# Performance work log

Measured on AMD Instinct MI355X. Metric: run time of the kernel, lower is better.

The kernel has to match this reference:

```python
import jax, jax.numpy as jnp
import numpy as np

B, H, W, C = 4, 64, 64, 256       # C == number_of_filters // 2
NOF = 512
CA = NOF // 8                      # f/g projection dim = 64
CH = NOF // 2                      # h / output projection dim = 256 (== C)


def setup_inputs() -> dict:
    key = jax.random.key(0)
    ks = jax.random.split(key, 10)
    sc = 1.0 / np.sqrt(C)
    x = jax.random.normal(ks[0], (B, H, W, C), jnp.float32)
    Wf = jax.random.normal(ks[1], (C, CA), jnp.float32) * sc
    bf = jnp.zeros((CA,), jnp.float32)
    Wg = jax.random.normal(ks[2], (C, CA), jnp.float32) * sc
    bg = jnp.zeros((CA,), jnp.float32)
    Wh = jax.random.normal(ks[3], (C, CH), jnp.float32) * sc
    bh = jnp.zeros((CH,), jnp.float32)
    Wo = jax.random.normal(ks[4], (CH, CH), jnp.float32) * (1.0 / np.sqrt(CH))
    bo = jnp.zeros((CH,), jnp.float32)
    gamma = jax.random.normal(ks[5], (1,), jnp.float32) * 0.1
    return {"x": x, "Wf": Wf, "bf": bf, "Wg": Wg, "bg": bg,
            "Wh": Wh, "bh": bh, "Wo": Wo, "bo": bo, "gamma": gamma}


def reference(x, Wf, bf, Wg, bg, Wh, bh, Wo, bo, gamma):
    b, h, w, c = x.shape
    n = h * w
    # 1x1 conv projections == per-pixel matmuls over channels
    f = (jnp.einsum('bhwc,cd->bhwd', x, Wf) + bf).reshape(b, n, -1)   # [B,N,CA]
    g = (jnp.einsum('bhwc,cd->bhwd', x, Wg) + bg).reshape(b, n, -1)   # [B,N,CA]
    hh = (jnp.einsum('bhwc,cd->bhwd', x, Wh) + bh).reshape(b, n, -1)  # [B,N,CH]
    # s = g @ f^T : full spatial attention scores [B,N,N]
    s = jnp.einsum('bnd,bmd->bnm', g, f)
    beta = jax.nn.softmax(s, axis=-1)
    o = jnp.einsum('bnm,bmc->bnc', beta, hh).reshape(b, h, w, c)      # CH == C
    # post-attention 1x1 conv
    o2 = jnp.einsum('bhwc,cd->bhwd', o, Wo) + bo
    y = gamma * o2 + x
    return y
```

## Files before the change

kernel.cpp:

```cpp
#include <hip/hip_runtime.h>

typedef __bf16  bf16x8 __attribute__((ext_vector_type(8)));
typedef short   s16x8  __attribute__((ext_vector_type(8)));
typedef float   f32x4  __attribute__((ext_vector_type(4)));
typedef float   f32x16 __attribute__((ext_vector_type(16)));
typedef int     i32x2  __attribute__((ext_vector_type(2)));
typedef int     i32x4  __attribute__((ext_vector_type(4)));

#define LOG2E 1.44269504088896f
#define SM_M2 (44.0f * LOG2E)

__device__ __forceinline__ unsigned short f2bf(float f){
  unsigned u = __builtin_bit_cast(unsigned, f);
  return (unsigned short)((u + 0x7fffu + ((u >> 16) & 1u)) >> 16);
}

__device__ __forceinline__ int cvtpk_bf16(float a, float b){
  int r; asm("v_cvt_pk_bf16_f32 %0, %1, %2" : "=v"(r) : "v"(a), "v"(b)); return r;
}

__device__ __forceinline__ float bfhalf2f(unsigned short u){
  unsigned v = ((unsigned)u) << 16; return __builtin_bit_cast(float, v);
}

#define OFF_WTFG 0u
#define OFF_WHT  65536u
#define OFF_WOT  196608u
#define OFF_F    8716288u
#define OFF_G    10813440u
#define OFF_HT   12910592u
#define OFF_PART 21299200u
#define OFF_LP   38076416u

__global__ __launch_bounds__(256) void prep(const float* __restrict__ Wf, const float* __restrict__ Wg,
                                            const float* __restrict__ Wh, const float* __restrict__ Wo,
                                            unsigned short* __restrict__ WTfg,
                                            unsigned short* __restrict__ WhT,
                                            unsigned short* __restrict__ WoT){
  int t = blockIdx.x * 256 + threadIdx.x;
  if (t < 32768) {
    int n = t >> 8, k = t & 255;
    float v = (n < 64) ? Wf[k * 64 + n] : Wg[k * 64 + (n - 64)];
    WTfg[t] = f2bf(v);
  } else if (t < 98304) {
    int i = t - 32768; int n = i >> 8, k = i & 255;
    WhT[i] = f2bf(Wh[k * 256 + n]);
  } else {
    int i = t - 98304; int n = i >> 8, k = i & 255;
    WoT[i] = f2bf(Wo[k * 256 + n]);
  }
}

__global__ __launch_bounds__(768) void proj(const float* __restrict__ x,
                                            const unsigned short* __restrict__ WTfg,
                                            const unsigned short* __restrict__ WhT,
                                            const float* __restrict__ bfv, const float* __restrict__ bgv,
                                            const float* __restrict__ bhv,
                                            unsigned short* __restrict__ fK, unsigned short* __restrict__ gQ,
                                            unsigned short* __restrict__ hT){
  __shared__ __attribute__((aligned(16))) char xt[32768];
  const int tid = threadIdx.x;
  const int lane = tid & 63, w = tid >> 6;
  const int l15 = lane & 15, g4 = lane >> 4;
  const int p0 = blockIdx.x * 64;

  for (int c = tid; c < 2048; c += 768) {
    int row = c >> 5, g = c & 31;
    const f32x4* gp = (const f32x4*)(x + (size_t)(p0 + row) * 256 + g * 8);
    f32x4 a = gp[0], bq = gp[1];
    i32x4 u;
    u[0] = cvtpk_bf16(a[0], a[1]);
    u[1] = cvtpk_bf16(a[2], a[3]);
    u[2] = cvtpk_bf16(bq[0], bq[1]);
    u[3] = cvtpk_bf16(bq[2], bq[3]);
    *(i32x4*)(xt + row * 512 + ((g ^ (row & 7)) << 4)) = u;
  }
  __syncthreads();

  auto XFRAG = [&](int pt, int kb) -> bf16x8 {
    int row = pt * 16 + l15;
    return *(const bf16x8*)(xt + row * 512 + (((kb * 4 + g4) ^ (row & 7)) << 4));
  };

  if (w < 4) {
#pragma unroll
    for (int j = 0; j < 2; j++) {
      int ctg = w * 2 + j, c0 = ctg * 16;
      bf16x8 bw[8];
      const unsigned short* wr = WTfg + (c0 + l15) * 256 + g4 * 8;
#pragma unroll
      for (int kb = 0; kb < 8; kb++) bw[kb] = *(const bf16x8*)(wr + kb * 32);
      float bias = (ctg < 4) ? bfv[c0 + l15] : bgv[c0 - 64 + l15];
      unsigned short* outp = (ctg < 4) ? (fK + c0 + l15) : (gQ + (c0 - 64) + l15);
#pragma unroll
      for (int pt = 0; pt < 4; pt++) {
        f32x4 acc = {0.f, 0.f, 0.f, 0.f};
#pragma unroll
        for (int kb = 0; kb < 8; kb++)
          acc = __builtin_amdgcn_mfma_f32_16x16x32_bf16(XFRAG(pt, kb), bw[kb], acc, 0, 0, 0);
#pragma unroll
        for (int r = 0; r < 4; r++) {
          int row = p0 + pt * 16 + g4 * 4 + r;
          outp[row * 64] = f2bf(acc[r] + bias);
        }
      }
    }
  } else {
#pragma unroll
    for (int j = 0; j < 2; j++) {
      int c0 = ((w - 4) * 2 + j) * 16;
      bf16x8 a[8];
      const unsigned short* wr = WhT + (c0 + l15) * 256 + g4 * 8;
#pragma unroll
      for (int kb = 0; kb < 8; kb++) a[kb] = *(const bf16x8*)(wr + kb * 32);
#pragma unroll
      for (int pt = 0; pt < 4; pt++) {
        f32x4 acc = {0.f, 0.f, 0.f, 0.f};
#pragma unroll
        for (int kb = 0; kb < 8; kb++)
          acc = __builtin_amdgcn_mfma_f32_16x16x32_bf16(a[kb], XFRAG(pt, kb), acc, 0, 0, 0);
        int pg = p0 + pt * 16;
        int bq = pg >> 12, n0 = pg & 4095;
        unsigned short* op = hT + bq * (256 * 4096) + n0 + l15;
#pragma unroll
        for (int r = 0; r < 4; r++) {
          int c = c0 + g4 * 4 + r;
          op[c * 4096] = f2bf(acc[r] + bhv[c]);
        }
      }
    }
  }
}

__global__ __launch_bounds__(512, 2) void attn1(const unsigned short* __restrict__ fK,
                                                const unsigned short* __restrict__ gQ,
                                                const unsigned short* __restrict__ hT,
                                                unsigned short* __restrict__ part,
                                                float* __restrict__ lpart){
  __shared__ __attribute__((aligned(16))) char smem[81920];
  const int tid  = threadIdx.x;
  const int lane = tid & 63, w = tid >> 6;
  const int l31  = lane & 31, hi = lane >> 5;
  const int qh   = w >> 1, cs = w & 1;
  const int b    = blockIdx.x & 3;
  const int rest = blockIdx.x >> 2;
  const int qb   = rest >> 1;
  const int kh   = rest & 1;
  const int q0   = qb * 128 + qh * 32;
  const int kbase = kh * 2048;

  const unsigned short* fKb = fK + (size_t)b * 4096 * 64;
  const unsigned short* gQb = gQ + (size_t)b * 4096 * 64;
  const unsigned short* hTb = hT + (size_t)b * 256 * 4096;

  bf16x8 qfr[4];
#pragma unroll
  for (int c4 = 0; c4 < 4; c4++)
    qfr[c4] = *(const bf16x8*)(gQb + (size_t)(q0 + l31) * 64 + c4 * 16 + hi * 8);

  char* buf0 = smem;
  char* buf1 = smem + 32768;
  char* kb0  = smem + 65536;
  char* kb1  = smem + 73728;

  auto STAGE = [&](char* vbuf, char* kbuf, int m0){
    int r = lane >> 3, gl = lane & 7;
#pragma unroll
    for (int k = 0; k < 4; k++){
      int c = 32 * w + k * 8 + r;
      const unsigned short* gp = hTb + (size_t)c * 4096 + m0 + ((gl ^ (c & 7)) * 8);
      __builtin_amdgcn_global_load_lds((const __attribute__((address_space(1))) unsigned int*)gp,
          (__attribute__((address_space(3))) unsigned int*)(vbuf + ((4 * w + k) << 10)), 16, 0, 0);
    }
    {
      int row = 8 * w + r;
      const unsigned short* gp = fKb + (size_t)(m0 + row) * 64 + ((gl ^ r) * 8);
      __builtin_amdgcn_global_load_lds((const __attribute__((address_space(1))) unsigned int*)gp,
          (__attribute__((address_space(3))) unsigned int*)(kbuf + (w << 10)), 16, 0, 0);
    }
  };

  f32x16 acc[4];
#pragma unroll
  for (int ct = 0; ct < 4; ct++)
#pragma unroll
    for (int i = 0; i < 16; i++) acc[ct][i] = 0.f;
  float lvec[16];
#pragma unroll
  for (int i = 0; i < 16; i++) lvec[i] = 0.f;

  auto COMPUTE = [&](const char* kbuf, const char* vbuf){
    bf16x8 Kf[8];
#pragma unroll
    for (int s = 0; s < 2; s++)
#pragma unroll
      for (int c4 = 0; c4 < 4; c4++)
        Kf[s * 4 + c4] = *(const bf16x8*)(kbuf + (s * 32 + l31) * 128 + (((c4 * 2 + hi) ^ (l31 & 7)) << 4));

    f32x16 t0 = {0,0,0,0,0,0,0,0,0,0,0,0,0,0,0,0};
    f32x16 t1 = {0,0,0,0,0,0,0,0,0,0,0,0,0,0,0,0};
#pragma unroll
    for (int c4 = 0; c4 < 4; c4++) t0 = __builtin_amdgcn_mfma_f32_32x32x16_bf16(Kf[c4],     qfr[c4], t0, 0, 0, 0);
#pragma unroll
    for (int c4 = 0; c4 < 4; c4++) t1 = __builtin_amdgcn_mfma_f32_32x32x16_bf16(Kf[4 + c4], qfr[c4], t1, 0, 0, 0);

    float p[32];
#pragma unroll
    for (int r = 0; r < 16; r++) p[r]      = __builtin_amdgcn_exp2f(fmaf(t0[r], LOG2E, -SM_M2));
#pragma unroll
    for (int r = 0; r < 16; r++) p[16 + r] = __builtin_amdgcn_exp2f(fmaf(t1[r], LOG2E, -SM_M2));
#pragma unroll
    for (int r = 0; r < 16; r++) lvec[r] += p[r] + p[16 + r];

    bf16x8 Bf[4];
#pragma unroll
    for (int mc = 0; mc < 4; mc++) {
      int x0 = cvtpk_bf16(p[mc*8+0], p[mc*8+1]);
      int x1 = cvtpk_bf16(p[mc*8+2], p[mc*8+3]);
      int y0 = cvtpk_bf16(p[mc*8+4], p[mc*8+5]);
      int y1 = cvtpk_bf16(p[mc*8+6], p[mc*8+7]);
      int b0, b1, b2, b3;
#if __has_builtin(__builtin_amdgcn_permlane32_swap)
      i32x2 r0 = __builtin_amdgcn_permlane32_swap(x0, y0, false, false);
      i32x2 r1 = __builtin_amdgcn_permlane32_swap(x1, y1, false, false);
      b0 = r0[0]; b1 = r1[0]; b2 = r0[1]; b3 = r1[1];
#else
      int xs0 = __shfl_xor(x0, 32), xs1 = __shfl_xor(x1, 32);
      int ys0 = __shfl_xor(y0, 32), ys1 = __shfl_xor(y1, 32);
      b0 = hi ? ys0 : x0;  b1 = hi ? ys1 : x1;
      b2 = hi ? y0  : xs0; b3 = hi ? y1  : xs1;
#endif
      union { int i[4]; bf16x8 v; } u;
      u.i[0] = b0; u.i[1] = b1; u.i[2] = b2; u.i[3] = b3;
      Bf[mc] = u.v;
    }

#pragma unroll
    for (int mc = 0; mc < 4; mc++) {
#pragma unroll
      for (int ct = 0; ct < 4; ct++) {
        int c = cs * 128 + ct * 32 + l31;
        const char* vp = vbuf + c * 128 + ((((mc * 2 + hi)) ^ (c & 7)) << 4);
        bf16x8 vf = *(const bf16x8*)vp;
        acc[ct] = __builtin_amdgcn_mfma_f32_32x32x16_bf16(vf, Bf[mc], acc[ct], 0, 0, 0);
      }
    }
  };

  STAGE(buf0, kb0, kbase);

  for (int it = 0; it < 32; it += 2) {
    STAGE(buf1, kb1, kbase + (it + 1) * 64);
    asm volatile("s_waitcnt vmcnt(5)" ::: "memory");
    __builtin_amdgcn_sched_barrier(0);
    __builtin_amdgcn_s_barrier();
    __builtin_amdgcn_sched_barrier(0);
    COMPUTE(kb0, buf0);
    __builtin_amdgcn_s_barrier();
    if (it + 2 < 32) {
      STAGE(buf0, kb0, kbase + (it + 2) * 64);
      asm volatile("s_waitcnt vmcnt(5)" ::: "memory");
    } else {
      asm volatile("s_waitcnt vmcnt(0)" ::: "memory");
    }
    __builtin_amdgcn_sched_barrier(0);
    __builtin_amdgcn_s_barrier();
    __builtin_amdgcn_sched_barrier(0);
    COMPUTE(kb1, buf1);
    __builtin_amdgcn_s_barrier();
  }

  float l_part = 0.f;
#pragma unroll
  for (int r = 0; r < 16; r++) l_part += lvec[r];
  l_part += __shfl_xor(l_part, 32);

  size_t tile = (size_t)((b * 32 + qb) * 2 + kh);
  if (cs == 0 && hi == 0)
    lpart[tile * 128 + qh * 32 + l31] = l_part;

  unsigned short* pbase = part + tile * (128 * 256);
  char* obase = smem;
#pragma unroll 1
  for (int ch = 0; ch < 4; ch++) {
    __syncthreads();
    if (qh == ch) {
      int q = l31;
#pragma unroll
      for (int ct = 0; ct < 4; ct++)
#pragma unroll
        for (int r = 0; r < 16; r += 2) {
          int c = cs * 128 + ct * 32 + 8 * (r >> 2) + 4 * hi + (r & 3);
          int u = cvtpk_bf16(acc[ct][r], acc[ct][r + 1]);
          int cb = c * 2;
          *(int*)(obase + q * 512 + (((cb >> 4) ^ (q & 7)) << 4) + (cb & 15)) = u;
        }
    }
    __syncthreads();
    int qq = tid >> 4, i = tid & 15;
#pragma unroll
    for (int j = 0; j < 2; j++) {
      int g = i * 2 + j;
      s16x8 v = *(const s16x8*)(obase + qq * 512 + ((g ^ (qq & 7)) << 4));
      *(s16x8*)(pbase + (ch * 32 + qq) * 256 + g * 8) = v;
    }
  }
}

__global__ __launch_bounds__(256, 2) void merge(const unsigned short* __restrict__ part,
                                                const float* __restrict__ lpart,
                                                const unsigned short* __restrict__ WoT,
                                                const float* __restrict__ bov,
                                                const float* __restrict__ gamma,
                                                const float* __restrict__ x,
                                                float* __restrict__ y){
  __shared__ __attribute__((aligned(16))) char obase[16384];
  const int tid  = threadIdx.x;
  const int lane = tid & 63, w = tid >> 6;
  const int b    = blockIdx.x & 3;
  const int rest = blockIdx.x >> 2;
  const int qb   = rest >> 2;
  const int off  = (rest & 3) * 32;

  size_t t0i = (size_t)((b * 32 + qb) * 2 + 0);
  size_t t1i = t0i + 1;
  const unsigned short* p0 = part + t0i * (128 * 256) + (size_t)off * 256;
  const unsigned short* p1 = part + t1i * (128 * 256) + (size_t)off * 256;

  {
    int q = tid >> 3, i = tid & 7;
    float inv = 1.0f / (lpart[t0i * 128 + off + q] + lpart[t1i * 128 + off + q]);
#pragma unroll
    for (int j = 0; j < 4; j++) {
      int c0 = i * 32 + j * 8;
      s16x8 v1 = *(const s16x8*)(p0 + q * 256 + c0);
      s16x8 v2 = *(const s16x8*)(p1 + q * 256 + c0);
#pragma unroll
      for (int k = 0; k < 4; k++) {
        float a0 = (bfhalf2f((unsigned short)v1[2*k])   + bfhalf2f((unsigned short)v2[2*k]))   * inv;
        float a1 = (bfhalf2f((unsigned short)v1[2*k+1]) + bfhalf2f((unsigned short)v2[2*k+1])) * inv;
        int c = c0 + 2 * k;
        int u = cvtpk_bf16(a0, a1);
        int cb = c * 2;
        *(int*)(obase + q * 512 + (((cb >> 4) ^ (q & 7)) << 4) + (cb & 15)) = u;
      }
    }
  }
  __syncthreads();
  {
    int l15 = lane & 15, g4 = lane >> 4;
    int q0e = (w & 1) * 16;
    int hf  = w >> 1;
    bf16x8 a[8];
    const char* orl = obase + (size_t)(q0e + l15) * 512;
#pragma unroll
    for (int kb = 0; kb < 8; kb++)
      a[kb] = *(const bf16x8*)(orl + (((kb * 4 + g4) ^ (l15 & 7)) << 4));
    float gm = gamma[0];
#pragma unroll
    for (int ct = 0; ct < 8; ct++) {
      int c0 = hf * 128 + ct * 16;
      f32x4 accp = {0.f, 0.f, 0.f, 0.f};
      const unsigned short* wr = WoT + (c0 + l15) * 256 + g4 * 8;
#pragma unroll
      for (int kb = 0; kb < 8; kb++) {
        bf16x8 bfr = *(const bf16x8*)(wr + kb * 32);
        accp = __builtin_amdgcn_mfma_f32_16x16x32_bf16(a[kb], bfr, accp, 0, 0, 0);
      }
      float bias = bov[c0 + l15];
#pragma unroll
      for (int r = 0; r < 4; r++) {
        int row = (b << 12) + qb * 128 + off + q0e + g4 * 4 + r;
        size_t idx = (size_t)row * 256 + c0 + l15;
        y[idx] = gm * (accp[r] + bias) + x[idx];
      }
    }
  }
}

extern "C" void kernel_launch(void* const* d_in, const int* in_sizes, int n_in,
                              void* d_out, int out_size, void* d_ws, size_t ws_size,
                              hipStream_t stream){
  const float* x     = (const float*)d_in[0];
  const float* Wf    = (const float*)d_in[1];
  const float* bfv   = (const float*)d_in[2];
  const float* Wg    = (const float*)d_in[3];
  const float* bgv   = (const float*)d_in[4];
  const float* Wh    = (const float*)d_in[5];
  const float* bhv   = (const float*)d_in[6];
  const float* Wo    = (const float*)d_in[7];
  const float* bov   = (const float*)d_in[8];
  const float* gamma = (const float*)d_in[9];
  float* y = (float*)d_out;

  char* ws = (char*)d_ws;
  unsigned short* WTfg = (unsigned short*)(ws + OFF_WTFG);
  unsigned short* WhT  = (unsigned short*)(ws + OFF_WHT);
  unsigned short* WoT  = (unsigned short*)(ws + OFF_WOT);
  unsigned short* fK   = (unsigned short*)(ws + OFF_F);
  unsigned short* gQ   = (unsigned short*)(ws + OFF_G);
  unsigned short* hT   = (unsigned short*)(ws + OFF_HT);
  unsigned short* part = (unsigned short*)(ws + OFF_PART);
  float*          lp   = (float*)(ws + OFF_LP);

  prep <<<640, 256, 0, stream>>>(Wf, Wg, Wh, Wo, WTfg, WhT, WoT);
  proj <<<256, 768, 0, stream>>>(x, WTfg, WhT, bfv, bgv, bhv, fK, gQ, hT);
  attn1<<<256, 512, 0, stream>>>(fK, gQ, hT, part, lp);
  merge<<<512, 256, 0, stream>>>(part, lp, WoT, bov, gamma, x, y);
}
```

Measured before the change: 105.2 us.

## Split attention key tile across wave pairs with 1024-thread blocks and LDS reduction

Doubles the attn1 block to 16 waves and splits each 64-key tile between two waves (ks), so each wave does half the QK, exp and PV work per step. The two partial accumulators and row sums are reduced through LDS in the epilogue before the bf16 partial output is written. Staging is split so waves 0-7 load V and waves 8-15 load K, with per-wave waitcnt adjusted. This aims to raise latency hiding and per-CU parallelism, at the cost of an extra fp32 LDS reduction, more barriers, and register pressure under a 1024-thread launch bound.

```diff
diff --git a/kernel.cpp b/kernel.cpp
--- a/kernel.cpp
+++ b/kernel.cpp
@@ -132,16 +132,18 @@
   }
 }
 
-__global__ __launch_bounds__(512, 2) void attn1(const unsigned short* __restrict__ fK,
-                                                const unsigned short* __restrict__ gQ,
-                                                const unsigned short* __restrict__ hT,
-                                                unsigned short* __restrict__ part,
-                                                float* __restrict__ lpart){
+__global__ __launch_bounds__(1024) void attn1(const unsigned short* __restrict__ fK,
+                                              const unsigned short* __restrict__ gQ,
+                                              const unsigned short* __restrict__ hT,
+                                              unsigned short* __restrict__ part,
+                                              float* __restrict__ lpart){
   __shared__ __attribute__((aligned(16))) char smem[81920];
   const int tid  = threadIdx.x;
   const int lane = tid & 63, w = tid >> 6;
   const int l31  = lane & 31, hi = lane >> 5;
-  const int qh   = w >> 1, cs = w & 1;
+  const int qh   = w >> 2;
+  const int cs   = (w >> 1) & 1;
+  const int ks   = w & 1;
   const int b    = blockIdx.x & 3;
   const int rest = blockIdx.x >> 2;
   const int qb   = rest >> 1;
@@ -164,19 +166,22 @@
   char* kb1  = smem + 73728;
 
   auto STAGE = [&](char* vbuf, char* kbuf, int m0){
-    int r = lane >> 3, gl = lane & 7;
-#pragma unroll
-    for (int k = 0; k < 4; k++){
-      int c = 32 * w + k * 8 + r;
-      const unsigned short* gp = hTb + (size_t)c * 4096 + m0 + ((gl ^ (c & 7)) * 8);
-      __builtin_amdgcn_global_load_lds((const __attribute__((address_space(1))) unsigned int*)gp,
-          (__attribute__((address_space(3))) unsigned int*)(vbuf + ((4 * w + k) << 10)), 16, 0, 0);
-    }
-    {
-      int row = 8 * w + r;
+    if (w < 8) {
+      int r = lane >> 3, gl = lane & 7;
+#pragma unroll
+      for (int k = 0; k < 4; k++){
+        int c = 32 * w + k * 8 + r;
+        const unsigned short* gp = hTb + (size_t)c * 4096 + m0 + ((gl ^ (c & 7)) * 8);
+        __builtin_amdgcn_global_load_lds((const __attribute__((address_space(1))) unsigned int*)gp,
+            (__attribute__((address_space(3))) unsigned int*)(vbuf + ((4 * w + k) << 10)), 16, 0, 0);
+      }
+    } else {
+      int r = lane >> 3, gl = lane & 7;
+      int w8 = w - 8;
+      int row = 8 * w8 + r;
       const unsigned short* gp = fKb + (size_t)(m0 + row) * 64 + ((gl ^ r) * 8);
       __builtin_amdgcn_global_load_lds((const __attribute__((address_space(1))) unsigned int*)gp,
-          (__attribute__((address_space(3))) unsigned int*)(kbuf + (w << 10)), 16, 0, 0);
+          (__attribute__((address_space(3))) unsigned int*)(kbuf + (w8 << 10)), 16, 0, 0);
     }
   };
 
@@ -190,31 +195,24 @@
   for (int i = 0; i < 16; i++) lvec[i] = 0.f;
 
   auto COMPUTE = [&](const char* kbuf, const char* vbuf){
-    bf16x8 Kf[8];
-#pragma unroll
-    for (int s = 0; s < 2; s++)
-#pragma unroll
-      for (int c4 = 0; c4 < 4; c4++)
-        Kf[s * 4 + c4] = *(const bf16x8*)(kbuf + (s * 32 + l31) * 128 + (((c4 * 2 + hi) ^ (l31 & 7)) << 4));
+    bf16x8 Kf[4];
+#pragma unroll
+    for (int c4 = 0; c4 < 4; c4++)
+      Kf[c4] = *(const bf16x8*)(kbuf + (ks * 32 + l31) * 128 + (((c4 * 2 + hi) ^ (l31 & 7)) << 4));
 
     f32x16 t0 = {0,0,0,0,0,0,0,0,0,0,0,0,0,0,0,0};
-    f32x16 t1 = {0,0,0,0,0,0,0,0,0,0,0,0,0,0,0,0};
-#pragma unroll
-    for (int c4 = 0; c4 < 4; c4++) t0 = __builtin_amdgcn_mfma_f32_32x32x16_bf16(Kf[c4],     qfr[c4], t0, 0, 0, 0);
-#pragma unroll
-    for (int c4 = 0; c4 < 4; c4++) t1 = __builtin_amdgcn_mfma_f32_32x32x16_bf16(Kf[4 + c4], qfr[c4], t1, 0, 0, 0);
-
-    float p[32];
-#pragma unroll
-    for (int r = 0; r < 16; r++) p[r]      = __builtin_amdgcn_exp2f(fmaf(t0[r], LOG2E, -SM_M2));
-#pragma unroll
-    for (int r = 0; r < 16; r++) p[16 + r] = __builtin_amdgcn_exp2f(fmaf(t1[r], LOG2E, -SM_M2));
-#pragma unroll
-    for (int r = 0; r < 16; r++) lvec[r] += p[r] + p[16 + r];
-
-    bf16x8 Bf[4];
-#pragma unroll
-    for (int mc = 0; mc < 4; mc++) {
+#pragma unroll
+    for (int c4 = 0; c4 < 4; c4++) t0 = __builtin_amdgcn_mfma_f32_32x32x16_bf16(Kf[c4], qfr[c4], t0, 0, 0, 0);
+
+    float p[16];
+#pragma unroll
+    for (int r = 0; r < 16; r++) p[r] = __builtin_amdgcn_exp2f(fmaf(t0[r], LOG2E, -SM_M2));
+#pragma unroll
+    for (int r = 0; r < 16; r++) lvec[r] += p[r];
+
+    bf16x8 Bf[2];
+#pragma unroll
+    for (int mc = 0; mc < 2; mc++) {
       int x0 = cvtpk_bf16(p[mc*8+0], p[mc*8+1]);
       int x1 = cvtpk_bf16(p[mc*8+2], p[mc*8+3]);
       int y0 = cvtpk_bf16(p[mc*8+4], p[mc*8+5]);
@@ -236,11 +234,11 @@
     }
 
 #pragma unroll
-    for (int mc = 0; mc < 4; mc++) {
+    for (int mc = 0; mc < 2; mc++) {
 #pragma unroll
       for (int ct = 0; ct < 4; ct++) {
         int c = cs * 128 + ct * 32 + l31;
-        const char* vp = vbuf + c * 128 + ((((mc * 2 + hi)) ^ (c & 7)) << 4);
+        const char* vp = vbuf + c * 128 + (((ks * 4 + mc * 2 + hi) ^ (c & 7)) << 4);
         bf16x8 vf = *(const bf16x8*)vp;
         acc[ct] = __builtin_amdgcn_mfma_f32_32x32x16_bf16(vf, Bf[mc], acc[ct], 0, 0, 0);
       }
@@ -251,7 +249,8 @@
 
   for (int it = 0; it < 32; it += 2) {
     STAGE(buf1, kb1, kbase + (it + 1) * 64);
-    asm volatile("s_waitcnt vmcnt(5)" ::: "memory");
+    if (w < 8) { asm volatile("s_waitcnt vmcnt(4)" ::: "memory"); }
+    else       { asm volatile("s_waitcnt vmcnt(1)" ::: "memory"); }
     __builtin_amdgcn_sched_barrier(0);
     __builtin_amdgcn_s_barrier();
     __builtin_amdgcn_sched_barrier(0);
@@ -259,7 +258,8 @@
     __builtin_amdgcn_s_barrier();
     if (it + 2 < 32) {
       STAGE(buf0, kb0, kbase + (it + 2) * 64);
-      asm volatile("s_waitcnt vmcnt(5)" ::: "memory");
+      if (w < 8) { asm volatile("s_waitcnt vmcnt(4)" ::: "memory"); }
+      else       { asm volatile("s_waitcnt vmcnt(1)" ::: "memory"); }
     } else {
       asm volatile("s_waitcnt vmcnt(0)" ::: "memory");
     }
@@ -276,33 +276,44 @@
   l_part += __shfl_xor(l_part, 32);
 
   size_t tile = (size_t)((b * 32 + qb) * 2 + kh);
-  if (cs == 0 && hi == 0)
-    lpart[tile * 128 + qh * 32 + l31] = l_part;
-
   unsigned short* pbase = part + tile * (128 * 256);
-  char* obase = smem;
+
+  float* smemF = (float*)smem;
+  char*  obase = smem + 40960;
 #pragma unroll 1
   for (int ch = 0; ch < 4; ch++) {
     __syncthreads();
-    if (qh == ch) {
-      int q = l31;
+    if (qh == ch && ks == 0) {
+#pragma unroll
+      for (int ct = 0; ct < 4; ct++)
+#pragma unroll
+        for (int r = 0; r < 16; r++) {
+          int c = cs * 128 + ct * 32 + 8 * (r >> 2) + 4 * hi + (r & 3);
+          smemF[l31 * 257 + c] = acc[ct][r];
+        }
+      if (cs == 0 && hi == 0) smemF[32 * 257 + l31] = l_part;
+    }
+    __syncthreads();
+    if (qh == ch && ks == 1) {
+      if (cs == 0 && hi == 0)
+        lpart[tile * 128 + ch * 32 + l31] = l_part + smemF[32 * 257 + l31];
 #pragma unroll
       for (int ct = 0; ct < 4; ct++)
 #pragma unroll
         for (int r = 0; r < 16; r += 2) {
           int c = cs * 128 + ct * 32 + 8 * (r >> 2) + 4 * hi + (r & 3);
-          int u = cvtpk_bf16(acc[ct][r], acc[ct][r + 1]);
+          float v0 = acc[ct][r]     + smemF[l31 * 257 + c];
+          float v1 = acc[ct][r + 1] + smemF[l31 * 257 + c + 1];
+          int u = cvtpk_bf16(v0, v1);
           int cb = c * 2;
-          *(int*)(obase + q * 512 + (((cb >> 4) ^ (q & 7)) << 4) + (cb & 15)) = u;
+          *(int*)(obase + l31 * 512 + (((cb >> 4) ^ (l31 & 7)) << 4) + (cb & 15)) = u;
         }
     }
     __syncthreads();
-    int qq = tid >> 4, i = tid & 15;
-#pragma unroll
-    for (int j = 0; j < 2; j++) {
-      int g = i * 2 + j;
-      s16x8 v = *(const s16x8*)(obase + qq * 512 + ((g ^ (qq & 7)) << 4));
-      *(s16x8*)(pbase + (ch * 32 + qq) * 256 + g * 8) = v;
+    {
+      int qq = tid >> 5, i = tid & 31;
+      s16x8 v = *(const s16x8*)(obase + qq * 512 + ((i ^ (qq & 7)) << 4));
+      *(s16x8*)(pbase + (ch * 32 + qq) * 256 + i * 8) = v;
     }
   }
 }
@@ -405,6 +416,6 @@
 
   prep <<<640, 256, 0, stream>>>(Wf, Wg, Wh, Wo, WTfg, WhT, WoT);
   proj <<<256, 768, 0, stream>>>(x, WTfg, WhT, bfv, bgv, bhv, fK, gQ, hT);
-  attn1<<<256, 512, 0, stream>>>(fK, gQ, hT, part, lp);
+  attn1<<<256, 1024, 0, stream>>>(fK, gQ, hT, part, lp);
   merge<<<512, 256, 0, stream>>>(part, lp, WoT, bov, gamma, x, y);
 }
```

Result: slower. 173.7 us (+65.2%).

## Software-pipeline PV matmul of previous tile with current QK scores

Applied to the files above, without the earlier changes.

Restructures the attention loop so each iteration computes QK^T scores for the current key tile while issuing the P·V MFMAs for the previous tile, using a triple-buffered LDS ring (prev/cur/next). The aim is to overlap exp/convert work with the PV MFMAs and cut dependency stalls. It raises LDS use from 80KB to 120KB per block, which may reduce occupancy under launch_bounds(512,2). It also drops the 2x manual unroll in favour of rotating pointers, which may cost some scheduling freedom.

```diff
diff --git a/kernel.cpp b/kernel.cpp
--- a/kernel.cpp
+++ b/kernel.cpp
@@ -137,7 +137,7 @@
                                                 const unsigned short* __restrict__ hT,
                                                 unsigned short* __restrict__ part,
                                                 float* __restrict__ lpart){
-  __shared__ __attribute__((aligned(16))) char smem[81920];
+  __shared__ __attribute__((aligned(16))) char smem[122880];
   const int tid  = threadIdx.x;
   const int lane = tid & 63, w = tid >> 6;
   const int l31  = lane & 31, hi = lane >> 5;
@@ -158,10 +158,12 @@
   for (int c4 = 0; c4 < 4; c4++)
     qfr[c4] = *(const bf16x8*)(gQb + (size_t)(q0 + l31) * 64 + c4 * 16 + hi * 8);
 
-  char* buf0 = smem;
-  char* buf1 = smem + 32768;
-  char* kb0  = smem + 65536;
-  char* kb1  = smem + 73728;
+  char* vPrv = smem + 65536;
+  char* vCur = smem;
+  char* vNxt = smem + 32768;
+  char* kPrv = smem + 114688;
+  char* kCur = smem + 98304;
+  char* kNxt = smem + 106496;
 
   auto STAGE = [&](char* vbuf, char* kbuf, int m0){
     int r = lane >> 3, gl = lane & 7;
@@ -188,8 +190,22 @@
   float lvec[16];
 #pragma unroll
   for (int i = 0; i < 16; i++) lvec[i] = 0.f;
-
-  auto COMPUTE = [&](const char* kbuf, const char* vbuf){
+  bf16x8 Bprev[4];
+
+  auto PVPREV = [&](const char* vprev){
+#pragma unroll
+    for (int mc = 0; mc < 4; mc++) {
+#pragma unroll
+      for (int ct = 0; ct < 4; ct++) {
+        int c = cs * 128 + ct * 32 + l31;
+        const char* vp = vprev + c * 128 + ((((mc * 2 + hi)) ^ (c & 7)) << 4);
+        bf16x8 vf = *(const bf16x8*)vp;
+        acc[ct] = __builtin_amdgcn_mfma_f32_32x32x16_bf16(vf, Bprev[mc], acc[ct], 0, 0, 0);
+      }
+    }
+  };
+
+  auto COMPUTE = [&](const char* kbuf, const char* vprev, int doPV){
     bf16x8 Kf[8];
 #pragma unroll
     for (int s = 0; s < 2; s++)
@@ -204,6 +220,8 @@
 #pragma unroll
     for (int c4 = 0; c4 < 4; c4++) t1 = __builtin_amdgcn_mfma_f32_32x32x16_bf16(Kf[4 + c4], qfr[c4], t1, 0, 0, 0);
 
+    if (doPV) PVPREV(vprev);
+
     float p[32];
 #pragma unroll
     for (int r = 0; r < 16; r++) p[r]      = __builtin_amdgcn_exp2f(fmaf(t0[r], LOG2E, -SM_M2));
@@ -212,7 +230,6 @@
 #pragma unroll
     for (int r = 0; r < 16; r++) lvec[r] += p[r] + p[16 + r];
 
-    bf16x8 Bf[4];
 #pragma unroll
     for (int mc = 0; mc < 4; mc++) {
       int x0 = cvtpk_bf16(p[mc*8+0], p[mc*8+1]);
@@ -232,43 +249,28 @@
 #endif
       union { int i[4]; bf16x8 v; } u;
       u.i[0] = b0; u.i[1] = b1; u.i[2] = b2; u.i[3] = b3;
-      Bf[mc] = u.v;
-    }
-
-#pragma unroll
-    for (int mc = 0; mc < 4; mc++) {
-#pragma unroll
-      for (int ct = 0; ct < 4; ct++) {
-        int c = cs * 128 + ct * 32 + l31;
-        const char* vp = vbuf + c * 128 + ((((mc * 2 + hi)) ^ (c & 7)) << 4);
-        bf16x8 vf = *(const bf16x8*)vp;
-        acc[ct] = __builtin_amdgcn_mfma_f32_32x32x16_bf16(vf, Bf[mc], acc[ct], 0, 0, 0);
-      }
+      Bprev[mc] = u.v;
     }
   };
 
-  STAGE(buf0, kb0, kbase);
-
-  for (int it = 0; it < 32; it += 2) {
-    STAGE(buf1, kb1, kbase + (it + 1) * 64);
-    asm volatile("s_waitcnt vmcnt(5)" ::: "memory");
+  STAGE(vCur, kCur, kbase);
+
+  for (int it = 0; it < 32; ++it) {
+    if (it + 1 < 32) {
+      STAGE(vNxt, kNxt, kbase + (it + 1) * 64);
+      asm volatile("s_waitcnt vmcnt(5)" ::: "memory");
+    } else {
+      asm volatile("s_waitcnt vmcnt(0)" ::: "memory");
+    }
     __builtin_amdgcn_sched_barrier(0);
     __builtin_amdgcn_s_barrier();
     __builtin_amdgcn_sched_barrier(0);
-    COMPUTE(kb0, buf0);
+    COMPUTE(kCur, vPrv, it != 0);
     __builtin_amdgcn_s_barrier();
-    if (it + 2 < 32) {
-      STAGE(buf0, kb0, kbase + (it + 2) * 64);
-      asm volatile("s_waitcnt vmcnt(5)" ::: "memory");
-    } else {
-      asm volatile("s_waitcnt vmcnt(0)" ::: "memory");
-    }
-    __builtin_amdgcn_sched_barrier(0);
-    __builtin_amdgcn_s_barrier();
-    __builtin_amdgcn_sched_barrier(0);
-    COMPUTE(kb1, buf1);
-    __builtin_amdgcn_s_barrier();
-  }
+    char* tv = vPrv; vPrv = vCur; vCur = vNxt; vNxt = tv;
+    char* tk = kPrv; kPrv = kCur; kCur = kNxt; kNxt = tk;
+  }
+  PVPREV(vPrv);
 
   float l_part = 0.f;
 #pragma unroll
```

Measured after the change: 108.6 us. 1.03x slower.
